# Optimization experiments

Hardware: AMD Instinct MI355X
Metric: run time of the kernel (lower is better)

## Reference

```python
import jax, jax.numpy as jnp
import numpy as np

D_MODEL = 1024
N_LAYERS = 2
D_STATE = 16
D_CONV = 4
D_INNER = 2 * D_MODEL          # mamba expand=2
DT_RANK = 64                   # ceil(d_model/16)
EPS = 1e-5


def rmsnorm(x, w, eps=EPS):
    return x * jax.lax.rsqrt(jnp.mean(x * x, axis=-1, keepdims=True) + eps) * w


def silu(x):
    return x * jax.nn.sigmoid(x)


def selective_scan(u, dt, A, B, C, Dp):
    # u, dt: (b,l,d)  A: (d,n)  B,C: (b,l,n)  Dp: (d,)
    b, l, d = u.shape
    n = A.shape[1]

    def step(h, inp):
        u_t, dt_t, B_t, C_t = inp          # (b,d),(b,d),(b,n),(b,n)
        dA = jnp.exp(dt_t[..., None] * A)  # (b,d,n)
        h = dA * h + (dt_t * u_t)[..., None] * B_t[:, None, :]
        y = jnp.einsum('bdn,bn->bd', h, C_t)
        return h, y

    h0 = jnp.zeros((b, d, n), u.dtype)
    xs = (u.transpose(1, 0, 2), dt.transpose(1, 0, 2),
          B.transpose(1, 0, 2), C.transpose(1, 0, 2))
    _, ys = jax.lax.scan(step, h0, xs)
    return ys.transpose(1, 0, 2) + u * Dp


def mamba_mixer(x, in_w, conv_w, conv_b, xp_w, dt_w, dt_b, A_log, Dp, out_w):
    b, l, _ = x.shape
    xz = jnp.einsum('bld,ed->ble', x, in_w)        # (b,l,2*d_inner)
    xi, z = jnp.split(xz, 2, axis=-1)
    # depthwise causal conv1d, kernel D_CONV
    xp = jnp.pad(xi, ((0, 0), (D_CONV - 1, 0), (0, 0)))
    xc = conv_b + sum(xp[:, k:k + l, :] * conv_w[:, k] for k in range(D_CONV))
    xc = silu(xc)
    dbc = jnp.einsum('bld,ed->ble', xc, xp_w)      # (b,l,dt_rank+2n)
    dt_low = dbc[..., :DT_RANK]
    Bm = dbc[..., DT_RANK:DT_RANK + D_STATE]
    Cm = dbc[..., DT_RANK + D_STATE:]
    dt = jax.nn.softplus(jnp.einsum('blr,dr->bld', dt_low, dt_w) + dt_b)
    A = -jnp.exp(A_log)
    y = selective_scan(xc, dt, A, Bm, Cm, Dp)
    y = y * silu(z)
    return jnp.einsum('bld,od->blo', y, out_w)


def setup_inputs() -> dict:
    key = jax.random.key(0)
    ks = jax.random.split(key, 8)
    s = 0.02
    hidden_states = jax.random.normal(ks[0], (1, 2048, D_MODEL), jnp.float32)
    norm_w = jnp.ones((N_LAYERS, D_MODEL), jnp.float32)
    in_proj_w = jax.random.normal(ks[1], (N_LAYERS, 2 * D_INNER, D_MODEL), jnp.float32) * s
    conv_w = jax.random.normal(ks[2], (N_LAYERS, D_INNER, D_CONV), jnp.float32) * 0.2
    conv_b = jnp.zeros((N_LAYERS, D_INNER), jnp.float32)
    x_proj_w = jax.random.normal(ks[3], (N_LAYERS, DT_RANK + 2 * D_STATE, D_INNER), jnp.float32) * s
    dt_proj_w = jax.random.normal(ks[4], (N_LAYERS, D_INNER, DT_RANK), jnp.float32) * (DT_RANK ** -0.5)
    # softplus^{-1}(0.01) ~= -4.6 (mamba dt bias init regime)
    dt_proj_b = jnp.full((N_LAYERS, D_INNER), -4.6, jnp.float32) + \
        jax.random.normal(ks[5], (N_LAYERS, D_INNER), jnp.float32) * 0.1
    A_log = jnp.log(jnp.broadcast_to(
        jnp.arange(1, D_STATE + 1, dtype=jnp.float32), (N_LAYERS, D_INNER, D_STATE)))
    D_param = jnp.ones((N_LAYERS, D_INNER), jnp.float32)
    out_proj_w = jax.random.normal(ks[6], (N_LAYERS, D_MODEL, D_INNER), jnp.float32) * s
    norm_f_w = jnp.ones((D_MODEL,), jnp.float32)
    return {
        'hidden_states': hidden_states, 'norm_w': norm_w, 'in_proj_w': in_proj_w,
        'conv_w': conv_w, 'conv_b': conv_b, 'x_proj_w': x_proj_w,
        'dt_proj_w': dt_proj_w, 'dt_proj_b': dt_proj_b, 'A_log': A_log,
        'D_param': D_param, 'out_proj_w': out_proj_w, 'norm_f_w': norm_f_w,
    }


def reference(hidden_states, norm_w, in_proj_w, conv_w, conv_b, x_proj_w,
              dt_proj_w, dt_proj_b, A_log, D_param, out_proj_w, norm_f_w):
    h = hidden_states
    residual = None
    for i in range(N_LAYERS):
        # fused add + RMSNorm (prenorm): residual accumulates the stream
        residual = h if residual is None else h + residual
        hn = rmsnorm(residual, norm_w[i])
        h = mamba_mixer(hn, in_proj_w[i], conv_w[i], conv_b[i], x_proj_w[i],
                        dt_proj_w[i], dt_proj_b[i], A_log[i], D_param[i], out_proj_w[i])
    # final fused add + RMSNorm (prenorm=False)
    return rmsnorm(h + residual, norm_f_w)
```

## Files before the change

kernel.cpp:

```cpp
#include <hip/hip_runtime.h>
#include <math.h>

#define D_MODEL 1024
#define D_INNER 2048
#define DPROJ   96
#define DT_RANK 64
#define NSTATE  16
#define SEQ     2048
#define CL      16
#define NCH     (SEQ/CL)
#define SCAN_SEGS 4
#define SCAN_CPS  (NCH / SCAN_SEGS)
#define LOG2E   1.44269504088896340736f

typedef unsigned short ushort_t;
typedef short v8s __attribute__((ext_vector_type(8)));
typedef float v4f __attribute__((ext_vector_type(4)));
typedef __attribute__((address_space(3))) unsigned int as3_u32;
typedef __attribute__((address_space(1))) unsigned int as1_u32;

__device__ __forceinline__ float silu_f(float x) { return x / (1.f + expf(-x)); }

__device__ __forceinline__ ushort_t f2bf(float f) {
  union { float f; unsigned u; } x; x.f = f;
  unsigned r = x.u + 0x7fffu + ((x.u >> 16) & 1u);
  return (ushort_t)(r >> 16);
}
__device__ __forceinline__ float bf2f(ushort_t b) {
  union { unsigned u; float f; } x; x.u = ((unsigned)b) << 16; return x.f;
}

__device__ __forceinline__ void gl_lds16(const ushort_t* g, ushort_t* l) {
  __builtin_amdgcn_global_load_lds((const as1_u32*)g, (as3_u32*)l, 16, 0, 0);
}

__global__ __launch_bounds__(256) void addrms_kernel(
    const float* __restrict__ a, const float* __restrict__ a2,
    const float* __restrict__ a3, const float* __restrict__ a4,
    const float* __restrict__ b,
    const float* __restrict__ w, float* __restrict__ res_out,
    float* __restrict__ xnf, ushort_t* __restrict__ xnb) {
  int t = blockIdx.x;
  int tid = threadIdx.x;
  float v[4];
  float ss = 0.f;
#pragma unroll
  for (int j = 0; j < 4; ++j) {
    int dcol = tid + j * 256;
    size_t off = (size_t)t * D_MODEL + dcol;
    float x = a[off];
    if (a2) x += a2[off];
    if (a3) x += a3[off];
    if (a4) x += a4[off];
    if (b) x += b[off];
    v[j] = x;
    ss += x * x;
  }
#pragma unroll
  for (int off = 32; off > 0; off >>= 1) ss += __shfl_down(ss, off);
  __shared__ float red[4];
  __shared__ float rmsv;
  int wid = tid >> 6, lane = tid & 63;
  if (lane == 0) red[wid] = ss;
  __syncthreads();
  if (tid == 0) {
    float s = red[0] + red[1] + red[2] + red[3];
    rmsv = rsqrtf(s / (float)D_MODEL + 1e-5f);
  }
  __syncthreads();
  float r = rmsv;
#pragma unroll
  for (int j = 0; j < 4; ++j) {
    int dcol = tid + j * 256;
    if (res_out) res_out[(size_t)t * D_MODEL + dcol] = v[j];
    float xn = v[j] * r * w[dcol];
    if (xnf) xnf[(size_t)t * D_MODEL + dcol] = xn;
    if (xnb) xnb[(size_t)t * D_MODEL + dcol] = f2bf(xn);
  }
}

__global__ __launch_bounds__(256) void f2bf_all_kernel(
    const float* __restrict__ s0, ushort_t* __restrict__ d0, int n0,
    const float* __restrict__ s1, ushort_t* __restrict__ d1, int n1,
    const float* __restrict__ s2, ushort_t* __restrict__ d2, int n2,
    const float* __restrict__ s3, ushort_t* __restrict__ d3, int n3) {
  int j = blockIdx.x * 256 + threadIdx.x;
  const float* s; ushort_t* d;
  if (j < n0) { s = s0; d = d0; }
  else {
    j -= n0;
    if (j < n1) { s = s1; d = d1; }
    else {
      j -= n1;
      if (j < n2) { s = s2; d = d2; }
      else {
        j -= n2;
        if (j >= n3) return;
        s = s3; d = d3;
      }
    }
  }
  float4 v = ((const float4*)s)[j];
  ushort4 o;
  o.x = f2bf(v.x); o.y = f2bf(v.y); o.z = f2bf(v.z); o.w = f2bf(v.w);
  ((ushort4*)d)[j] = o;
}

template <int SPLITK, bool CLAMPN, int EPI>
__global__ __launch_bounds__(256) void gemm_bt(
    const ushort_t* __restrict__ A, const ushort_t* __restrict__ B,
    void* __restrict__ Cv, const float* __restrict__ bias,
    const ushort_t* __restrict__ upack,
    int M, int N, int K, int lda, int ldb, int ldc) {
  __shared__ ushort_t As[2][128 * 32];
  __shared__ ushort_t Bs[2][128 * 32];
  int tid = threadIdx.x;
  int bm = blockIdx.y * 128;
  int bn = blockIdx.x * 128;
  int kchunk = K / SPLITK;
  int k0 = blockIdx.z * kchunk;
  int nk = kchunk / 32;

  int lane = tid & 63, wid = tid >> 6;
  int wr = wid >> 1, wc = wid & 1;
  int lr = lane & 15;
  int ko = (lane >> 4) * 8;

  int rs0 = wid * 16 + (lane >> 2);
  int segc = (lane & 3) * 8;

  auto stage = [&](int buf, int kt) {
#pragma unroll
    for (int s = 0; s < 2; ++s) {
      int r = s * 64 + rs0;
      int cc = kt + segc;
      gl_lds16(A + (size_t)(bm + r) * lda + cc, &As[buf][s * 2048 + wid * 512]);
      int bc = bn + r;
      if (CLAMPN) bc = min(bc, N - 1);
      gl_lds16(B + (size_t)bc * ldb + cc, &Bs[buf][s * 2048 + wid * 512]);
    }
  };

  v4f acc[4][4] = {};

  stage(0, k0);
  __syncthreads();
  int cur = 0;
  for (int it = 0; it < nk; ++it) {
    if (it + 1 < nk) stage(cur ^ 1, k0 + (it + 1) * 32);
    v8s a[4], b[4];
#pragma unroll
    for (int m = 0; m < 4; ++m)
      a[m] = *(const v8s*)&As[cur][(wr * 64 + m * 16 + lr) * 32 + ko];
#pragma unroll
    for (int n = 0; n < 4; ++n)
      b[n] = *(const v8s*)&Bs[cur][(wc * 64 + n * 16 + lr) * 32 + ko];
#pragma unroll
    for (int m = 0; m < 4; ++m)
#pragma unroll
      for (int n = 0; n < 4; ++n)
        acc[m][n] = __builtin_amdgcn_mfma_f32_16x16x32_bf16(a[m], b[n], acc[m][n], 0, 0, 0);
    __syncthreads();
    cur ^= 1;
  }

  float* Cf = (float*)Cv;
  ushort_t* Cb = (ushort_t*)Cv;
  unsigned* Cu = (unsigned*)Cv;
  if (SPLITK > 1) Cf += (size_t)blockIdx.z * (size_t)M * (size_t)ldc;

#pragma unroll
  for (int m = 0; m < 4; ++m) {
#pragma unroll
    for (int n = 0; n < 4; ++n) {
      int gc = bn + wc * 64 + n * 16 + lr;
      if (gc >= N) continue;
      int gr0 = bm + wr * 64 + m * 16 + (lane >> 4) * 4;
      float bv = (EPI == 1 || EPI == 3) ? bias[gc] : 0.f;
#pragma unroll
      for (int j = 0; j < 4; ++j) {
        float val = acc[m][n][j];
        size_t idx = (size_t)(gr0 + j) * ldc + gc;
        if (EPI == 0) {
          Cf[idx] = val;
        } else if (EPI == 1) {
          float x = val + bv;
          x = fmaxf(x, 0.f) + log1pf(expf(-fabsf(x)));
          Cb[idx] = f2bf(x);
        } else if (EPI == 2) {
          Cb[idx] = f2bf(val);
        } else {
          float x = val + bv;
          x = fmaxf(x, 0.f) + log1pf(expf(-fabsf(x)));
          Cu[idx] = (unsigned)f2bf(x) | ((unsigned)upack[idx] << 16);
        }
      }
    }
  }
}

__global__ __launch_bounds__(256) void reduceN_kernel(
    const float* __restrict__ part, float* __restrict__ out,
    ushort_t* __restrict__ outb, int sz, int nparts) {
  int idx = blockIdx.x * 256 + threadIdx.x;
  if (idx >= sz) return;
  float s = 0.f;
  for (int p = 0; p < nparts; ++p) s += part[idx + (size_t)p * sz];
  out[idx] = s;
  if (outb) outb[idx] = f2bf(s);
}

__global__ __launch_bounds__(256) void conv_silu_kernel(
    const ushort_t* __restrict__ xzb, const float* __restrict__ cw,
    const float* __restrict__ cb, ushort_t* __restrict__ xcb) {
  int idx = blockIdx.x * 256 + threadIdx.x;
  int t = idx >> 9;
  int c = (idx & 511) * 4;
  float acc[4];
  float4 cbv = *(const float4*)&cb[c];
  acc[0] = cbv.x; acc[1] = cbv.y; acc[2] = cbv.z; acc[3] = cbv.w;
  float4 wv[4];
#pragma unroll
  for (int i = 0; i < 4; ++i) wv[i] = *(const float4*)&cw[(c + i) * 4];
#pragma unroll
  for (int k = 0; k < 4; ++k) {
    int ts = t - 3 + k;
    if (ts < 0) continue;
    ushort4 x = *(const ushort4*)&xzb[(size_t)ts * 4096 + c];
    acc[0] = fmaf(bf2f(x.x), ((const float*)&wv[0])[k], acc[0]);
    acc[1] = fmaf(bf2f(x.y), ((const float*)&wv[1])[k], acc[1]);
    acc[2] = fmaf(bf2f(x.z), ((const float*)&wv[2])[k], acc[2]);
    acc[3] = fmaf(bf2f(x.w), ((const float*)&wv[3])[k], acc[3]);
  }
  ushort4 o;
  o.x = f2bf(silu_f(acc[0]));
  o.y = f2bf(silu_f(acc[1]));
  o.z = f2bf(silu_f(acc[2]));
  o.w = f2bf(silu_f(acc[3]));
  *(ushort4*)&xcb[(size_t)t * D_INNER + c] = o;
}

__global__ __launch_bounds__(256) void scan_passA_kernel(
    const unsigned* __restrict__ dtu, const float* __restrict__ dbc,
    const float* __restrict__ A_log,
    float* __restrict__ aprod, float* __restrict__ hend) {
  __shared__ float Bsh[CL][16];
  int c = blockIdx.x;
  int d = blockIdx.y * 256 + threadIdx.x;
  int t0 = c * CL;
  {
    int j = threadIdx.x;
    if (j < CL * 4) {
      int r = j >> 2, col = (j & 3) * 4;
      *(float4*)&Bsh[r][col] = *(const float4*)&dbc[(size_t)(t0 + r) * DPROJ + DT_RANK + col];
    }
  }
  float Av[NSTATE], h[NSTATE], ap[NSTATE];
#pragma unroll
  for (int n = 0; n < NSTATE; ++n) {
    Av[n] = -expf(A_log[(size_t)d * NSTATE + n]) * LOG2E;
    h[n] = 0.f;
    ap[n] = 1.f;
  }
  __syncthreads();
#pragma unroll 2
  for (int tt = 0; tt < CL; ++tt) {
    unsigned p = dtu[(size_t)(t0 + tt) * D_INNER + d];
    float dtv = bf2f((ushort_t)(p & 0xffffu));
    float uv  = bf2f((ushort_t)(p >> 16));
    float du = dtv * uv;
#pragma unroll
    for (int n = 0; n < NSTATE; ++n) {
      float dA = exp2f(dtv * Av[n]);
      h[n] = fmaf(dA, h[n], du * Bsh[tt][n]);
      ap[n] *= dA;
    }
  }
  size_t base = ((size_t)c * D_INNER + d) * NSTATE;
#pragma unroll
  for (int n = 0; n < NSTATE; ++n) {
    aprod[base + n] = ap[n];
    hend[base + n] = h[n];
  }
}

__global__ __launch_bounds__(256) void scan_passB_kernel(
    const float* __restrict__ aprod, float* __restrict__ hend_hin) {
  int tid = threadIdx.x;
  int lane = tid & 63;
  int wave = tid >> 6;
  int seg = lane >> 4;
  int chain = blockIdx.x * 64 + wave * 16 + (lane & 15);
  const size_t stride = (size_t)D_INNER * NSTATE;
  float a[SCAN_CPS], e[SCAN_CPS];
  float P = 1.f, E = 0.f;
  int c0 = seg * SCAN_CPS;
#pragma unroll
  for (int j = 0; j < SCAN_CPS; ++j) {
    a[j] = aprod[(size_t)(c0 + j) * stride + chain];
    e[j] = hend_hin[(size_t)(c0 + j) * stride + chain];
    E = fmaf(a[j], E, e[j]);
    P *= a[j];
  }
#pragma unroll
  for (int dstep = 1; dstep < SCAN_SEGS; dstep <<= 1) {
    float Pp = __shfl_up(P, dstep * 16);
    float Ep = __shfl_up(E, dstep * 16);
    if (seg >= dstep) { E = fmaf(P, Ep, E); P *= Pp; }
  }
  float Ex = __shfl_up(E, 16);
  if (seg == 0) Ex = 0.f;
  float h = Ex;
#pragma unroll
  for (int j = 0; j < SCAN_CPS; ++j) {
    hend_hin[(size_t)(c0 + j) * stride + chain] = h;
    h = fmaf(a[j], h, e[j]);
  }
}

__global__ __launch_bounds__(256) void scan_passC_kernel(
    const unsigned* __restrict__ dtu, const float* __restrict__ dbc,
    const float* __restrict__ A_log, const float* __restrict__ Dp,
    const ushort_t* __restrict__ xzb, const float* __restrict__ hin,
    ushort_t* __restrict__ yb) {
  __shared__ float BCsh[CL][32];
  int c = blockIdx.x;
  int d = blockIdx.y * 256 + threadIdx.x;
  int t0 = c * CL;
  {
    int j = threadIdx.x;
    if (j < CL * 8) {
      int r = j >> 3, col = (j & 7) * 4;
      *(float4*)&BCsh[r][col] = *(const float4*)&dbc[(size_t)(t0 + r) * DPROJ + DT_RANK + col];
    }
  }
  float Av[NSTATE], h[NSTATE];
  size_t base = ((size_t)c * D_INNER + d) * NSTATE;
#pragma unroll
  for (int n = 0; n < NSTATE; ++n) {
    Av[n] = -expf(A_log[(size_t)d * NSTATE + n]) * LOG2E;
    h[n] = hin[base + n];
  }
  float Dv = Dp[d];
  __syncthreads();
#pragma unroll 2
  for (int tt = 0; tt < CL; ++tt) {
    unsigned p = dtu[(size_t)(t0 + tt) * D_INNER + d];
    float dtv = bf2f((ushort_t)(p & 0xffffu));
    float uv  = bf2f((ushort_t)(p >> 16));
    float du = dtv * uv;
    float yv = 0.f;
#pragma unroll
    for (int n = 0; n < NSTATE; ++n) {
      float dA = exp2f(dtv * Av[n]);
      h[n] = fmaf(dA, h[n], du * BCsh[tt][n]);
      yv = fmaf(h[n], BCsh[tt][16 + n], yv);
    }
    float zv = bf2f(xzb[(size_t)(t0 + tt) * 4096 + D_INNER + d]);
    yb[(size_t)(t0 + tt) * D_INNER + d] = f2bf((yv + uv * Dv) * silu_f(zv));
  }
}

extern "C" void kernel_launch(void* const* d_in, const int* in_sizes, int n_in,
                              void* d_out, int out_size, void* d_ws, size_t ws_size,
                              hipStream_t stream) {
  const float* h_in   = (const float*)d_in[0];
  const float* norm_w = (const float*)d_in[1];
  const float* in_w   = (const float*)d_in[2];
  const float* conv_w = (const float*)d_in[3];
  const float* conv_b = (const float*)d_in[4];
  const float* xp_w   = (const float*)d_in[5];
  const float* dt_w   = (const float*)d_in[6];
  const float* dt_b   = (const float*)d_in[7];
  const float* A_log  = (const float*)d_in[8];
  const float* Dp     = (const float*)d_in[9];
  const float* out_w  = (const float*)d_in[10];
  const float* normf  = (const float*)d_in[11];
  float* out = (float*)d_out;

  float* ws = (float*)d_ws;
  const size_t TD = (size_t)SEQ * D_MODEL;
  const size_t TI = (size_t)SEQ * D_INNER;
  const size_t ST = (size_t)NCH * D_INNER * NSTATE;
  const size_t DB = (size_t)SEQ * DPROJ;
  const size_t INW = (size_t)2 * D_INNER * D_MODEL;
  const size_t XPW = (size_t)DPROJ * D_INNER;
  const size_t DTW = (size_t)D_INNER * DT_RANK;
  const size_t OUW = (size_t)D_MODEL * D_INNER;

  float* res   = ws; ws += TD;
  float* dbc   = ws; ws += DB;
  float* pk    = ws; ws += ST;
  float* hend  = ws; ws += ST;
  unsigned* dtu = (unsigned*)ws; ws += TI;
  ushort_t* hnb  = (ushort_t*)ws;
  ushort_t* xzb  = hnb + TD;
  ushort_t* xcb  = xzb + 2 * TI;
  ushort_t* ybf  = xcb + TI;
  ushort_t* dbcb = ybf + TI;
  ushort_t* inwb = dbcb + DB;
  ushort_t* xpwb = inwb + 2 * INW;
  ushort_t* dtwb = xpwb + 2 * XPW;
  ushort_t* ouwb = dtwb + 2 * DTW;

  {
    int n0 = (int)(2 * INW / 4), n1 = (int)(2 * XPW / 4);
    int n2 = (int)(2 * DTW / 4), n3 = (int)(2 * OUW / 4);
    int tot = n0 + n1 + n2 + n3;
    f2bf_all_kernel<<<(tot + 255) / 256, 256, 0, stream>>>(
        in_w, inwb, n0, xp_w, xpwb, n1, dt_w, dtwb, n2, out_w, ouwb, n3);
  }

  for (int i = 0; i < 2; ++i) {
    addrms_kernel<<<SEQ, 256, 0, stream>>>(
        i == 0 ? h_in : pk,
        i == 0 ? nullptr : pk + TD,
        i == 0 ? nullptr : pk + 2 * TD,
        i == 0 ? nullptr : pk + 3 * TD,
        i == 0 ? nullptr : res,
        norm_w + (size_t)i * D_MODEL, res, nullptr, hnb);
    gemm_bt<1, false, 2><<<dim3(32, 16, 1), 256, 0, stream>>>(
        hnb, inwb + (size_t)i * INW, xzb, nullptr, nullptr,
        SEQ, 2 * D_INNER, D_MODEL, D_MODEL, D_MODEL, 2 * D_INNER);
    conv_silu_kernel<<<(int)(TI / 4 / 256), 256, 0, stream>>>(
        xzb, conv_w + (size_t)i * D_INNER * 4, conv_b + (size_t)i * D_INNER, xcb);
    gemm_bt<16, true, 0><<<dim3(1, 16, 16), 256, 0, stream>>>(
        xcb, xpwb + (size_t)i * XPW, pk, nullptr, nullptr,
        SEQ, DPROJ, D_INNER, D_INNER, D_INNER, DPROJ);
    reduceN_kernel<<<(DB + 255) / 256, 256, 0, stream>>>(pk, dbc, dbcb, (int)DB, 16);
    gemm_bt<1, false, 3><<<dim3(16, 16, 1), 256, 0, stream>>>(
        dbcb, dtwb + (size_t)i * DTW, dtu, dt_b + (size_t)i * D_INNER, xcb,
        SEQ, D_INNER, DT_RANK, DPROJ, DT_RANK, D_INNER);
    scan_passA_kernel<<<dim3(NCH, D_INNER / 256), 256, 0, stream>>>(
        dtu, dbc, A_log + (size_t)i * D_INNER * NSTATE, pk, hend);
    scan_passB_kernel<<<(D_INNER * NSTATE) / 64, 256, 0, stream>>>(pk, hend);
    scan_passC_kernel<<<dim3(NCH, D_INNER / 256), 256, 0, stream>>>(
        dtu, dbc, A_log + (size_t)i * D_INNER * NSTATE,
        Dp + (size_t)i * D_INNER, xzb, hend, ybf);
    gemm_bt<4, false, 0><<<dim3(8, 16, 4), 256, 0, stream>>>(
        ybf, ouwb + (size_t)i * OUW, pk, nullptr, nullptr,
        SEQ, D_MODEL, D_INNER, D_INNER, D_INNER, D_MODEL);
  }
  addrms_kernel<<<SEQ, 256, 0, stream>>>(
      pk, pk + TD, pk + 2 * TD, pk + 3 * TD, res, normf, nullptr, out, nullptr);
}
```

Measured before the change: 388.8 us.

## Fuse three-pass chunked selective scan into one cooperative kernel with grid syncs

Replaces the three scan kernels (per-chunk local scan, cross-chunk prefix, and output pass) with a single cooperative kernel of 512 blocks. Each block handles two chunks for 256 channels, keeps dt/u values in registers and B/C in shared memory, and uses grid.sync between phases. The aim is to remove two kernel launches and the re-reading of dt/u and B/C between passes. In exchange it needs the whole grid co-resident, holds a 32-element register array per thread that may raise register pressure, and adds grid-wide barrier cost. It falls back to the old three kernels if the cooperative launch fails.

```diff
diff --git a/kernel.cpp b/kernel.cpp
--- a/kernel.cpp
+++ b/kernel.cpp
@@ -1,4 +1,5 @@
 #include <hip/hip_runtime.h>
+#include <hip/hip_cooperative_groups.h>
 #include <math.h>
 
 #define D_MODEL 1024
@@ -358,6 +359,124 @@
     }
     float zv = bf2f(xzb[(size_t)(t0 + tt) * 4096 + D_INNER + d]);
     yb[(size_t)(t0 + tt) * D_INNER + d] = f2bf((yv + uv * Dv) * silu_f(zv));
+  }
+}
+
+__global__ __launch_bounds__(256, 2) void scan_fused_kernel(
+    const unsigned* __restrict__ dtu, const float* __restrict__ dbc,
+    const float* __restrict__ A_log, const float* __restrict__ Dp,
+    const ushort_t* __restrict__ xzb, float* __restrict__ aprod,
+    float* __restrict__ hend, ushort_t* __restrict__ yb) {
+  cooperative_groups::grid_group grid = cooperative_groups::this_grid();
+  int tid = threadIdx.x;
+  int cg = blockIdx.x >> 3;
+  int d = (blockIdx.x & 7) * 256 + tid;
+  __shared__ float BCsh[2][CL][32];
+  {
+    int j = tid;
+    int cc = j >> 7;
+    int r = (j >> 3) & 15;
+    int col = (j & 7) * 4;
+    int t0s = (cg * 2 + cc) * CL;
+    *(float4*)&BCsh[cc][r][col] =
+        *(const float4*)&dbc[(size_t)(t0s + r) * DPROJ + DT_RANK + col];
+  }
+  float Av[NSTATE];
+  unsigned dup[2][CL];
+#pragma unroll
+  for (int n = 0; n < NSTATE; ++n)
+    Av[n] = -expf(A_log[(size_t)d * NSTATE + n]) * LOG2E;
+  __syncthreads();
+
+#pragma unroll
+  for (int cc = 0; cc < 2; ++cc) {
+    int c = cg * 2 + cc;
+    int t0 = c * CL;
+    float h[NSTATE], ap[NSTATE];
+#pragma unroll
+    for (int n = 0; n < NSTATE; ++n) { h[n] = 0.f; ap[n] = 1.f; }
+#pragma unroll
+    for (int tt = 0; tt < CL; ++tt) {
+      unsigned p = dtu[(size_t)(t0 + tt) * D_INNER + d];
+      dup[cc][tt] = p;
+      float dtv = bf2f((ushort_t)(p & 0xffffu));
+      float uv  = bf2f((ushort_t)(p >> 16));
+      float du = dtv * uv;
+#pragma unroll
+      for (int n = 0; n < NSTATE; ++n) {
+        float dA = exp2f(dtv * Av[n]);
+        h[n] = fmaf(dA, h[n], du * BCsh[cc][tt][n]);
+        ap[n] *= dA;
+      }
+    }
+    size_t base = ((size_t)c * D_INNER + d) * NSTATE;
+#pragma unroll
+    for (int n = 0; n < NSTATE; ++n) {
+      aprod[base + n] = ap[n];
+      hend[base + n] = h[n];
+    }
+  }
+
+  grid.sync();
+
+  {
+    int lane = tid & 63, wave = tid >> 6;
+    int seg = lane >> 4;
+    int chain = blockIdx.x * 64 + wave * 16 + (lane & 15);
+    const size_t stride = (size_t)D_INNER * NSTATE;
+    float a[SCAN_CPS], e[SCAN_CPS];
+    float P = 1.f, E = 0.f;
+    int c0 = seg * SCAN_CPS;
+#pragma unroll
+    for (int j = 0; j < SCAN_CPS; ++j) {
+      a[j] = aprod[(size_t)(c0 + j) * stride + chain];
+      e[j] = hend[(size_t)(c0 + j) * stride + chain];
+      E = fmaf(a[j], E, e[j]);
+      P *= a[j];
+    }
+#pragma unroll
+    for (int dstep = 1; dstep < SCAN_SEGS; dstep <<= 1) {
+      float Pp = __shfl_up(P, dstep * 16);
+      float Ep = __shfl_up(E, dstep * 16);
+      if (seg >= dstep) { E = fmaf(P, Ep, E); P *= Pp; }
+    }
+    float Ex = __shfl_up(E, 16);
+    if (seg == 0) Ex = 0.f;
+    float hh = Ex;
+#pragma unroll
+    for (int j = 0; j < SCAN_CPS; ++j) {
+      hend[(size_t)(c0 + j) * stride + chain] = hh;
+      hh = fmaf(a[j], hh, e[j]);
+    }
+  }
+
+  grid.sync();
+
+  float Dv = Dp[d];
+#pragma unroll
+  for (int cc = 0; cc < 2; ++cc) {
+    int c = cg * 2 + cc;
+    int t0 = c * CL;
+    size_t base = ((size_t)c * D_INNER + d) * NSTATE;
+    float h[NSTATE];
+#pragma unroll
+    for (int n = 0; n < NSTATE; ++n) h[n] = hend[base + n];
+#pragma unroll
+    for (int tt = 0; tt < CL; ++tt) {
+      unsigned p = dup[cc][tt];
+      float dtv = bf2f((ushort_t)(p & 0xffffu));
+      float uv  = bf2f((ushort_t)(p >> 16));
+      float du = dtv * uv;
+      float yv = 0.f;
+#pragma unroll
+      for (int n = 0; n < NSTATE; ++n) {
+        float dA = exp2f(dtv * Av[n]);
+        h[n] = fmaf(dA, h[n], du * BCsh[cc][tt][n]);
+        yv = fmaf(h[n], BCsh[cc][tt][16 + n], yv);
+      }
+      float zv = bf2f(xzb[(size_t)(t0 + tt) * 4096 + D_INNER + d]);
+      yb[(size_t)(t0 + tt) * D_INNER + d] = f2bf((yv + uv * Dv) * silu_f(zv));
+    }
   }
 }
 
@@ -431,12 +550,25 @@
     gemm_bt<1, false, 3><<<dim3(16, 16, 1), 256, 0, stream>>>(
         dbcb, dtwb + (size_t)i * DTW, dtu, dt_b + (size_t)i * D_INNER, xcb,
         SEQ, D_INNER, DT_RANK, DPROJ, DT_RANK, D_INNER);
-    scan_passA_kernel<<<dim3(NCH, D_INNER / 256), 256, 0, stream>>>(
-        dtu, dbc, A_log + (size_t)i * D_INNER * NSTATE, pk, hend);
-    scan_passB_kernel<<<(D_INNER * NSTATE) / 64, 256, 0, stream>>>(pk, hend);
-    scan_passC_kernel<<<dim3(NCH, D_INNER / 256), 256, 0, stream>>>(
-        dtu, dbc, A_log + (size_t)i * D_INNER * NSTATE,
-        Dp + (size_t)i * D_INNER, xzb, hend, ybf);
+    {
+      const float* Ai = A_log + (size_t)i * D_INNER * NSTATE;
+      const float* Di = Dp + (size_t)i * D_INNER;
+      const unsigned* dtup = dtu;
+      const ushort_t* xzp = xzb;
+      float* pkp = pk; float* hep = hend; ushort_t* ybp = ybf;
+      const float* dbp = dbc;
+      void* args[] = { (void*)&dtup, (void*)&dbp, (void*)&Ai, (void*)&Di,
+                       (void*)&xzp, (void*)&pkp, (void*)&hep, (void*)&ybp };
+      hipError_t cerr = hipLaunchCooperativeKernel(
+          (void*)scan_fused_kernel, dim3(512), dim3(256), args, 0, stream);
+      if (cerr != hipSuccess) {
+        scan_passA_kernel<<<dim3(NCH, D_INNER / 256), 256, 0, stream>>>(
+            dtu, dbc, Ai, pk, hend);
+        scan_passB_kernel<<<(D_INNER * NSTATE) / 64, 256, 0, stream>>>(pk, hend);
+        scan_passC_kernel<<<dim3(NCH, D_INNER / 256), 256, 0, stream>>>(
+            dtu, dbc, Ai, Di, xzb, hend, ybf);
+      }
+    }
     gemm_bt<4, false, 0><<<dim3(8, 16, 4), 256, 0, stream>>>(
         ybf, ouwb + (size_t)i * OUW, pk, nullptr, nullptr,
         SEQ, D_MODEL, D_INNER, D_INNER, D_INNER, D_MODEL);
```

After: 1.037 ms. 2.67x slower.
